# Performance work log

Hardware: AMD Instinct MI355X
Metric: run time of the kernel (lower is better)

Reference implementation:

```python
import jax, jax.numpy as jnp
import numpy as np

LN_EPS = 1e-5


def layer_norm(x, g, b):
    mu = jnp.mean(x, axis=-1, keepdims=True)
    var = jnp.mean(jnp.square(x - mu), axis=-1, keepdims=True)
    return (x - mu) * jax.lax.rsqrt(var + LN_EPS) * g + b


def setup_inputs() -> dict:
    key = jax.random.key(0)
    ks = jax.random.split(key, 8)
    N, E, D = 100000, 1000000, 128
    node_feat = jax.random.normal(ks[0], (N, D), dtype=jnp.float32)
    edge_index = jax.random.randint(ks[1], (2, E), 0, N, dtype=jnp.int64)
    s = 1.0 / np.sqrt(D)
    return {
        "node_feat": node_feat,
        "edge_index": edge_index,
        "layer_idx": 0,
        "ln1_g": jnp.ones((D,), jnp.float32),
        "ln1_b": jnp.zeros((D,), jnp.float32),
        "W_conv": jax.random.normal(ks[2], (D, D), jnp.float32) * s,
        "b_conv": jnp.zeros((D,), jnp.float32),
        "ln2_g": jnp.ones((D,), jnp.float32),
        "ln2_b": jnp.zeros((D,), jnp.float32),
        "W1": jax.random.normal(ks[3], (D, 4 * D), jnp.float32) * s,
        "b1": jnp.zeros((4 * D,), jnp.float32),
        "W2": jax.random.normal(ks[4], (4 * D, D), jnp.float32) * (0.5 * s),
        "b2": jnp.zeros((D,), jnp.float32),
    }


def reference(node_feat, edge_index, layer_idx, ln1_g, ln1_b, W_conv, b_conv,
              ln2_g, ln2_b, W1, b1, W2, b2):
    N = node_feat.shape[0]
    # DeepGCNLayer block='res+': x + conv(dropout(act(norm(x)))); dropout inert at eval
    h = jax.nn.gelu(layer_norm(node_feat, ln1_g, ln1_b), approximate=False)
    # GCNConv: symmetric-normalized aggregation with added self-loops
    hW = h @ W_conv                                         # [N, D]
    loops = jnp.arange(N, dtype=edge_index.dtype)
    src = jnp.concatenate([edge_index[0], loops])           # [E+N]
    dst = jnp.concatenate([edge_index[1], loops])
    deg = jax.ops.segment_sum(jnp.ones(src.shape, hW.dtype), dst, num_segments=N)
    dinv = jnp.where(deg > 0, jax.lax.rsqrt(deg), 0.0)
    coef = dinv[src] * dinv[dst]                            # [E+N]
    agg = jax.ops.segment_sum(hW[src] * coef[:, None], dst, num_segments=N)
    conv_feat = node_feat + agg + b_conv
    # FFN: LN -> Linear(D,4D) -> GELU -> Linear(4D,D) -> GELU, residual from node_feat
    f = layer_norm(conv_feat, ln2_g, ln2_b)
    f = jax.nn.gelu(f @ W1 + b1, approximate=False)
    f = jax.nn.gelu(f @ W2 + b2, approximate=False)
    return node_feat + f
```

## Files before the change

kernel.cpp:

```cpp
#include <hip/hip_runtime.h>
#include <math.h>


typedef _Float16 half8  __attribute__((ext_vector_type(8)));
typedef _Float16 half2v __attribute__((ext_vector_type(2)));
typedef __fp16   fp16x2 __attribute__((ext_vector_type(2)));
typedef float    floatx4 __attribute__((ext_vector_type(4)));

#define SBLK 128

__device__ __forceinline__ float gelu_f(float x){
  float x2 = x*x;
  float z  = x*(1.5957691216f + 0.07135481283f*x2);
  float e  = __expf(-z);
  return x * __builtin_amdgcn_rcpf(1.0f + e);
}
__device__ __forceinline__ unsigned pk16(float a, float b){
  fp16x2 h = __builtin_amdgcn_cvt_pkrtz(a, b);
  return __builtin_bit_cast(unsigned, h);
}
__device__ __forceinline__ float wave_reduce_sum(float v){
  #pragma unroll
  for (int off = 32; off > 0; off >>= 1) v += __shfl_xor(v, off, 64);
  return v;
}

__global__ __launch_bounds__(256) void k_hist(const int* __restrict__ ei, int* __restrict__ cnt,
                                              int E, int NB, int ESB,
    const float* __restrict__ Wc, const float* __restrict__ W1, const float* __restrict__ W2,
    _Float16* __restrict__ Wcp, _Float16* __restrict__ W1p, _Float16* __restrict__ W2p,
    const float* __restrict__ nf, const float* __restrict__ g, const float* __restrict__ b,
    _Float16* __restrict__ hs)
{
  int bid = blockIdx.x;
  if (bid < SBLK){
    __shared__ int h[2048];
    int t = threadIdx.x;
    for (int i = t; i < NB; i += 256) h[i] = 0;
    __syncthreads();
    int e0 = bid * ESB;
    int e1 = min(E, e0 + ESB);
    for (int e = e0 + t; e < e1; e += 256)
      atomicAdd(&h[ei[E + e] >> 6], 1);
    __syncthreads();
    for (int i = t; i < NB; i += 256) cnt[(size_t)bid * NB + i] = h[i];
  } else if (bid < SBLK + 72){
    int id = (bid - SBLK)*256 + threadIdx.x;
    const float* W; _Float16* P; int K, Nc, base;
    if (id < 2048)            { W = Wc; P = Wcp; K = 128; Nc = 128; base = id; }
    else if (id < 2048+8192)  { W = W1; P = W1p; K = 128; Nc = 512; base = id - 2048; }
    else                      { W = W2; P = W2p; K = 512; Nc = 128; base = id - 10240; }
    int lane = base & 63;
    int nkb  = K >> 5;
    int kb   = (base >> 6) % nkb;
    int tile = base / (nkb << 6);
    int col  = (tile << 4) + (lane & 15);
    int k0   = (kb << 5) + ((lane >> 4) << 3);
    _Float16 v[8];
    #pragma unroll
    for (int j = 0; j < 8; j++) v[j] = (_Float16)W[(size_t)(k0 + j)*Nc + col];
    *(half8*)&P[(size_t)base * 8] = *(const half8*)v;
  } else {
    int w = threadIdx.x >> 6, l = threadIdx.x & 63;
    int node = (bid - SBLK - 72)*4 + w;
    float2 x = *(const float2*)&nf[(size_t)node*128 + 2*l];
    float mu = wave_reduce_sum(x.x + x.y) * 0.0078125f;
    float d0 = x.x - mu, d1 = x.y - mu;
    float var = wave_reduce_sum(d0*d0 + d1*d1) * 0.0078125f;
    float rs = rsqrtf(var + 1e-5f);
    float y0 = gelu_f(d0*rs*g[2*l]   + b[2*l]);
    float y1 = gelu_f(d1*rs*g[2*l+1] + b[2*l+1]);
    *(unsigned*)&hs[(size_t)node*128 + 2*l] = pk16(y0, y1);
  }
}

__global__ __launch_bounds__(128) void k_scanB(int* __restrict__ cnt, int* __restrict__ total,
                                               int NB){
  __shared__ int w0sum;
  int b = blockIdx.x;
  int t = threadIdx.x, l = t & 63, w = t >> 6;
  int v = cnt[(size_t)t*NB + b];
  int x = v;
  #pragma unroll
  for (int off = 1; off < 64; off <<= 1){
    int y = __shfl_up(x, off);
    if (l >= off) x += y;
  }
  if (w == 0 && l == 63) w0sum = x;
  __syncthreads();
  int ex = x - v + (w ? w0sum : 0);
  cnt[(size_t)t*NB + b] = ex;
  if (t == 127) total[b] = ex + v;
}

__global__ __launch_bounds__(256) void k_scan2(const int* __restrict__ total,
                                               int* __restrict__ bucketStart, int NB){
  __shared__ int wsum[4];
  int t = threadIdx.x, w = t >> 6, l = t & 63;
  int vals[8];
  int sum = 0;
  #pragma unroll
  for (int j = 0; j < 8; j++){
    int idx = t*8 + j;
    vals[j] = (idx < NB) ? total[idx] : 0;
    sum += vals[j];
  }
  int x = sum;
  #pragma unroll
  for (int off = 1; off < 64; off <<= 1){
    int y = __shfl_up(x, off);
    if (l >= off) x += y;
  }
  if (l == 63) wsum[w] = x;
  __syncthreads();
  if (t == 0){
    int s = 0;
    #pragma unroll
    for (int i = 0; i < 4; i++){ int c = wsum[i]; wsum[i] = s; s += c; }
  }
  __syncthreads();
  int run = wsum[w] + x - sum;
  #pragma unroll
  for (int j = 0; j < 8; j++){
    int idx = t*8 + j;
    if (idx < NB) bucketStart[idx] = run;
    run += vals[j];
  }
  if (t == 255) bucketStart[NB] = run;
}

__global__ __launch_bounds__(256) void k_scatter(const int* __restrict__ ei,
    const int* __restrict__ cnt, const int* __restrict__ bucketStart,
    int* __restrict__ eb, int E, int NB, int ESB){
  __shared__ int cur[2048];
  int t = threadIdx.x;
  for (int i = t; i < NB; i += 256)
    cur[i] = bucketStart[i] + cnt[(size_t)blockIdx.x*NB + i];
  __syncthreads();
  int e0 = blockIdx.x*ESB, e1 = min(E, e0 + ESB);
  for (int e = e0 + t; e < e1; e += 256){
    int s = ei[e], d = ei[E + e];
    int pos = atomicAdd(&cur[d >> 6], 1);
    eb[pos] = (s << 6) | (d & 63);
  }
}

__global__ __launch_bounds__(256) void k_sort2(const int* __restrict__ eb,
    const int* __restrict__ bucketStart, int* __restrict__ eSrc,
    int* __restrict__ row_start, int* __restrict__ incount,
    float* __restrict__ dinv, int N){
  __shared__ int hcnt[64];
  __shared__ int hcur[64];
  int b = blockIdx.x, t = threadIdx.x;
  if (t < 64) hcnt[t] = 0;
  __syncthreads();
  int s0 = bucketStart[b], s1 = bucketStart[b+1];
  for (int e = s0 + t; e < s1; e += 256) atomicAdd(&hcnt[eb[e] & 63], 1);
  __syncthreads();
  if (t < 64){
    int v = hcnt[t];
    int x = v;
    #pragma unroll
    for (int off = 1; off < 64; off <<= 1){
      int y = __shfl_up(x, off);
      if (t >= off) x += y;
    }
    int ex = x - v;
    hcur[t] = ex;
    int node = (b << 6) + t;
    if (node < N){
      row_start[node] = s0 + ex;
      incount[node]   = v;
      dinv[node]      = rsqrtf((float)v + 1.0f);
    }
  }
  __syncthreads();
  for (int e = s0 + t; e < s1; e += 256){
    int v = eb[e];
    int pos = atomicAdd(&hcur[v & 63], 1);
    eSrc[s0 + pos] = v >> 6;
  }
}

__global__ __launch_bounds__(256) void k_gather(const _Float16* __restrict__ hs,
    const int* __restrict__ eSrc, const int* __restrict__ row_start,
    const int* __restrict__ incount, const float* __restrict__ dinv,
    _Float16* __restrict__ aggh, int N)
{
  int w = threadIdx.x >> 6, l = threadIdx.x & 63;
  int node = (blockIdx.x << 2) + w;
  int g  = l >> 3;
  int li = l & 7;
  float dn = dinv[node];
  int start = row_start[node], cnt = incount[node];
  float acc[16];
  #pragma unroll
  for (int i = 0; i < 16; i++) acc[i] = 0.f;
  for (int e = g; e < cnt + 1; e += 8){
    int s = (e == 0) ? node : eSrc[start + e - 1];
    float ds = dinv[s];
    const uint4* hp = (const uint4*)&hs[(size_t)s*128 + (li << 4)];
    uint4 v0 = hp[0], v1 = hp[1];
    half2v p0 = __builtin_bit_cast(half2v, v0.x), p1 = __builtin_bit_cast(half2v, v0.y);
    half2v p2 = __builtin_bit_cast(half2v, v0.z), p3 = __builtin_bit_cast(half2v, v0.w);
    half2v p4 = __builtin_bit_cast(half2v, v1.x), p5 = __builtin_bit_cast(half2v, v1.y);
    half2v p6 = __builtin_bit_cast(half2v, v1.z), p7 = __builtin_bit_cast(half2v, v1.w);
    acc[0]  = fmaf((float)p0.x, ds, acc[0]);  acc[1]  = fmaf((float)p0.y, ds, acc[1]);
    acc[2]  = fmaf((float)p1.x, ds, acc[2]);  acc[3]  = fmaf((float)p1.y, ds, acc[3]);
    acc[4]  = fmaf((float)p2.x, ds, acc[4]);  acc[5]  = fmaf((float)p2.y, ds, acc[5]);
    acc[6]  = fmaf((float)p3.x, ds, acc[6]);  acc[7]  = fmaf((float)p3.y, ds, acc[7]);
    acc[8]  = fmaf((float)p4.x, ds, acc[8]);  acc[9]  = fmaf((float)p4.y, ds, acc[9]);
    acc[10] = fmaf((float)p5.x, ds, acc[10]); acc[11] = fmaf((float)p5.y, ds, acc[11]);
    acc[12] = fmaf((float)p6.x, ds, acc[12]); acc[13] = fmaf((float)p6.y, ds, acc[13]);
    acc[14] = fmaf((float)p7.x, ds, acc[14]); acc[15] = fmaf((float)p7.y, ds, acc[15]);
  }
  #pragma unroll
  for (int i = 0; i < 16; i++){
    acc[i] += __shfl_xor(acc[i], 8);
    acc[i] += __shfl_xor(acc[i], 16);
    acc[i] += __shfl_xor(acc[i], 32);
  }
  if (l < 8){
    uint4 o0, o1;
    o0.x = pk16(dn*acc[0],  dn*acc[1]);  o0.y = pk16(dn*acc[2],  dn*acc[3]);
    o0.z = pk16(dn*acc[4],  dn*acc[5]);  o0.w = pk16(dn*acc[6],  dn*acc[7]);
    o1.x = pk16(dn*acc[8],  dn*acc[9]);  o1.y = pk16(dn*acc[10], dn*acc[11]);
    o1.z = pk16(dn*acc[12], dn*acc[13]); o1.w = pk16(dn*acc[14], dn*acc[15]);
    uint4* op = (uint4*)&aggh[(size_t)node*128 + (l << 4)];
    op[0] = o0; op[1] = o1;
  }
}

__global__ __launch_bounds__(256) void k_ffn(
    const float* __restrict__ nf, const _Float16* __restrict__ aggh,
    const _Float16* __restrict__ Wcp, const float* __restrict__ bc,
    const float* __restrict__ g2, const float* __restrict__ bl2,
    const _Float16* __restrict__ W1p, const float* __restrict__ b1,
    const _Float16* __restrict__ W2p, const float* __restrict__ b2,
    float* __restrict__ out, int N)
{
  __shared__ __align__(16) unsigned short u_s[32*520];
  int t = threadIdx.x, w = t >> 6, l = t & 63;
  int nb = blockIdx.x << 5;
  int quad = l >> 4, ln16 = l & 15;

  {
    int m = t >> 3, c0 = (t & 7) << 4;
    const uint4* src = (const uint4*)&aggh[(size_t)(nb + m)*128 + c0];
    uint4 v0 = src[0], v1 = src[1];
    uint4* dst = (uint4*)&u_s[4352 + m*136 + c0];
    dst[0] = v0; dst[1] = v1;
  }
  __syncthreads();

  {
    half8 ag[2][4];
    #pragma unroll
    for (int mt = 0; mt < 2; mt++)
      #pragma unroll
      for (int kb = 0; kb < 4; kb++)
        ag[mt][kb] = *(const half8*)&u_s[4352 + ((mt << 4) + ln16)*136 + (kb << 5) + (quad << 3)];
    const half8* Wp8 = (const half8*)Wcp;
    #pragma unroll
    for (int nt = 0; nt < 2; nt++){
      int tile = (w << 1) + nt;
      half8 bf[4];
      #pragma unroll
      for (int kb = 0; kb < 4; kb++) bf[kb] = Wp8[(size_t)((tile << 2) + kb)*64 + l];
      floatx4 acc0 = {0.f,0.f,0.f,0.f}, acc1 = {0.f,0.f,0.f,0.f};
      #pragma unroll
      for (int kb = 0; kb < 4; kb++){
        acc0 = __builtin_amdgcn_mfma_f32_16x16x32_f16(ag[0][kb], bf[kb], acc0, 0, 0, 0);
        acc1 = __builtin_amdgcn_mfma_f32_16x16x32_f16(ag[1][kb], bf[kb], acc1, 0, 0, 0);
      }
      int col = (tile << 4) + ln16;
      float bcv = bc[col];
      #pragma unroll
      for (int r = 0; r < 4; r++){
        int m0 = (quad << 2) + r;
        *(_Float16*)&u_s[m0*136 + col]        = (_Float16)(acc0[r] + bcv);
        *(_Float16*)&u_s[(m0 + 16)*136 + col] = (_Float16)(acc1[r] + bcv);
      }
    }
  }
  __syncthreads();

  float2 nfr[8];
  #pragma unroll
  for (int q = 0; q < 8; q++){
    int m = (w << 3) + q;
    unsigned pu = *(unsigned*)&u_s[m*136 + 2*l];
    half2v hp = __builtin_bit_cast(half2v, pu);
    nfr[q] = *(const float2*)&nf[(size_t)(nb + m)*128 + 2*l];
    float x0 = (float)hp.x + nfr[q].x;
    float x1 = (float)hp.y + nfr[q].y;
    float mu = wave_reduce_sum(x0 + x1) * 0.0078125f;
    float d0 = x0 - mu, d1 = x1 - mu;
    float var = wave_reduce_sum(d0*d0 + d1*d1) * 0.0078125f;
    float rs = rsqrtf(var + 1e-5f);
    float y0 = d0*rs*g2[2*l]   + bl2[2*l];
    float y1 = d1*rs*g2[2*l+1] + bl2[2*l+1];
    *(unsigned*)&u_s[m*136 + 2*l] = pk16(y0, y1);
  }
  __syncthreads();

  half8 a[2][4];
  #pragma unroll
  for (int mt = 0; mt < 2; mt++)
    #pragma unroll
    for (int kb = 0; kb < 4; kb++)
      a[mt][kb] = *(const half8*)&u_s[((mt << 4) + ln16)*136 + (kb << 5) + (quad << 3)];
  __syncthreads();

  {
    const half8* Wp8 = (const half8*)W1p;
    #pragma unroll
    for (int nt = 0; nt < 8; nt++){
      int tile = (w << 3) + nt;
      half8 bf[4];
      #pragma unroll
      for (int kb = 0; kb < 4; kb++) bf[kb] = Wp8[(size_t)((tile << 2) + kb)*64 + l];
      floatx4 acc0 = {0.f,0.f,0.f,0.f}, acc1 = {0.f,0.f,0.f,0.f};
      #pragma unroll
      for (int kb = 0; kb < 4; kb++){
        acc0 = __builtin_amdgcn_mfma_f32_16x16x32_f16(a[0][kb], bf[kb], acc0, 0, 0, 0);
        acc1 = __builtin_amdgcn_mfma_f32_16x16x32_f16(a[1][kb], bf[kb], acc1, 0, 0, 0);
      }
      int col = (tile << 4) + ln16;
      float bv = b1[col];
      #pragma unroll
      for (int r = 0; r < 4; r++){
        *(_Float16*)&u_s[((quad << 2) + r)*520 + col]      = (_Float16)gelu_f(acc0[r] + bv);
        *(_Float16*)&u_s[(16 + (quad << 2) + r)*520 + col] = (_Float16)gelu_f(acc1[r] + bv);
      }
    }
  }
  __syncthreads();

  floatx4 acc00 = {0.f,0.f,0.f,0.f}, acc01 = {0.f,0.f,0.f,0.f};
  floatx4 acc10 = {0.f,0.f,0.f,0.f}, acc11 = {0.f,0.f,0.f,0.f};
  int tile0 = (w << 1), tile1 = tile0 + 1;
  {
    const half8* Wp8 = (const half8*)W2p;
    for (int kb = 0; kb < 16; kb++){
      half8 a0 = *(const half8*)&u_s[ln16*520        + (kb << 5) + (quad << 3)];
      half8 a1 = *(const half8*)&u_s[(16 + ln16)*520 + (kb << 5) + (quad << 3)];
      half8 b0  = Wp8[(size_t)((tile0 << 4) + kb)*64 + l];
      half8 b1v = Wp8[(size_t)((tile1 << 4) + kb)*64 + l];
      acc00 = __builtin_amdgcn_mfma_f32_16x16x32_f16(a0, b0,  acc00, 0, 0, 0);
      acc01 = __builtin_amdgcn_mfma_f32_16x16x32_f16(a0, b1v, acc01, 0, 0, 0);
      acc10 = __builtin_amdgcn_mfma_f32_16x16x32_f16(a1, b0,  acc10, 0, 0, 0);
      acc11 = __builtin_amdgcn_mfma_f32_16x16x32_f16(a1, b1v, acc11, 0, 0, 0);
    }
  }
  __syncthreads();

  {
    float* fs = (float*)u_s;
    int col0 = (tile0 << 4) + ln16, col1 = (tile1 << 4) + ln16;
    float bv0 = b2[col0], bv1 = b2[col1];
    #pragma unroll
    for (int r = 0; r < 4; r++){
      int m0 = (quad << 2) + r;
      fs[m0*132 + col0]        = gelu_f(acc00[r] + bv0);
      fs[m0*132 + col1]        = gelu_f(acc01[r] + bv1);
      fs[(m0 + 16)*132 + col0] = gelu_f(acc10[r] + bv0);
      fs[(m0 + 16)*132 + col1] = gelu_f(acc11[r] + bv1);
    }
  }
  __syncthreads();

  {
    const float* fs = (const float*)u_s;
    #pragma unroll
    for (int q = 0; q < 8; q++){
      int m = (w << 3) + q;
      float2 o;
      o.x = nfr[q].x + fs[m*132 + 2*l];
      o.y = nfr[q].y + fs[m*132 + 2*l + 1];
      *(float2*)&out[(size_t)(nb + m)*128 + 2*l] = o;
    }
  }
}

extern "C" void kernel_launch(void* const* d_in, const int* in_sizes, int n_in,
                              void* d_out, int out_size, void* d_ws, size_t ws_size,
                              hipStream_t stream) {
  const float* nf   = (const float*)d_in[0];
  const int*   ei   = (const int*)  d_in[1];
  const float* ln1g = (const float*)d_in[3];
  const float* ln1b = (const float*)d_in[4];
  const float* Wc   = (const float*)d_in[5];
  const float* bc   = (const float*)d_in[6];
  const float* ln2g = (const float*)d_in[7];
  const float* ln2b = (const float*)d_in[8];
  const float* W1   = (const float*)d_in[9];
  const float* b1   = (const float*)d_in[10];
  const float* W2   = (const float*)d_in[11];
  const float* b2   = (const float*)d_in[12];
  float* out = (float*)d_out;

  int N = in_sizes[0] / 128;
  int E = in_sizes[1] / 2;
  int NB  = (N + 63) >> 6;
  int ESB = (E + SBLK - 1) / SBLK;

  char* ws = (char*)d_ws;
  _Float16* hs   = (_Float16*)ws;
  _Float16* aggh = (_Float16*)(ws + (size_t)N*128*2);
  char* p = ws + (size_t)N*128*4;
  p = (char*)(((size_t)p + 15) & ~(size_t)15);
  int*   cnt         = (int*)p;   p += (size_t)SBLK*NB*4;
  int*   total       = (int*)p;   p += (size_t)NB*4;
  int*   bucketStart = (int*)p;   p += (size_t)(NB+1)*4;
  float* dinv        = (float*)p; p += (size_t)N*4;
  int*   incount     = (int*)p;   p += (size_t)N*4;
  int*   row_start   = (int*)p;   p += (size_t)N*4;
  int*   eb          = (int*)p;   p += (size_t)E*4;
  int*   eSrc        = (int*)p;   p += (size_t)E*4;
  p = (char*)(((size_t)p + 15) & ~(size_t)15);
  _Float16* Wcp = (_Float16*)p; p += (size_t)2048*8*2;
  _Float16* W1p = (_Float16*)p; p += (size_t)8192*8*2;
  _Float16* W2p = (_Float16*)p; p += (size_t)8192*8*2;

  k_hist   <<<SBLK + 72 + N/4, 256, 0, stream>>>(ei, cnt, E, NB, ESB,
                                                 Wc, W1, W2, Wcp, W1p, W2p,
                                                 nf, ln1g, ln1b, hs);
  k_scanB  <<<NB, 128, 0, stream>>>(cnt, total, NB);
  k_scan2  <<<1, 256, 0, stream>>>(total, bucketStart, NB);
  k_scatter<<<SBLK, 256, 0, stream>>>(ei, cnt, bucketStart, eb, E, NB, ESB);
  k_sort2  <<<NB, 256, 0, stream>>>(eb, bucketStart, eSrc, row_start, incount, dinv, N);

  k_gather <<<N/4, 256, 0, stream>>>(hs, eSrc, row_start, incount, dinv, aggh, N);
  k_ffn    <<<N/32, 256, 0, stream>>>(nf, aggh, Wcp, bc, ln2g, ln2b, W1p, b1, W2p, b2, out, N);
}
```

Measured before the change: 286.8 us.

## Spread LN1 node blocks across the sort-phase kernels to fill idle CUs

The LayerNorm+GELU work over the N/4 node blocks is split into four fixed chunks (4000/8000/5000/8000), each appended to one of the histogram, per-bucket scan, global scan and scatter kernels. Those small kernels otherwise leave most CUs idle. The per-bucket scan now handles two buckets per 256-thread block, and the weight-packing blocks move into that kernel. The chunk sizes are hardcoded and total exactly N/4 = 25000 for N=100000, so other N would leave nodes uncomputed or read out of range.

After: 289.7 us. Within noise of the previous version (+1.0%).

```diff
diff --git a/kernel.cpp b/kernel.cpp
--- a/kernel.cpp
+++ b/kernel.cpp
@@ -8,6 +8,10 @@
 typedef float    floatx4 __attribute__((ext_vector_type(4)));
 
 #define SBLK 128
+#define LN1_A 4000
+#define LN1_B 8000
+#define LN1_C 5000
+#define LN1_D 8000
 
 __device__ __forceinline__ float gelu_f(float x){
   float x2 = x*x;
@@ -25,10 +29,24 @@
   return v;
 }
 
-__global__ __launch_bounds__(256) void k_hist(const int* __restrict__ ei, int* __restrict__ cnt,
-                                              int E, int NB, int ESB,
-    const float* __restrict__ Wc, const float* __restrict__ W1, const float* __restrict__ W2,
-    _Float16* __restrict__ Wcp, _Float16* __restrict__ W1p, _Float16* __restrict__ W2p,
+__device__ __forceinline__ void ln1_body(int node_blk,
+    const float* __restrict__ nf, const float* __restrict__ g,
+    const float* __restrict__ b, _Float16* __restrict__ hs)
+{
+  int w = threadIdx.x >> 6, l = threadIdx.x & 63;
+  int node = node_blk*4 + w;
+  float2 x = *(const float2*)&nf[(size_t)node*128 + 2*l];
+  float mu = wave_reduce_sum(x.x + x.y) * 0.0078125f;
+  float d0 = x.x - mu, d1 = x.y - mu;
+  float var = wave_reduce_sum(d0*d0 + d1*d1) * 0.0078125f;
+  float rs = rsqrtf(var + 1e-5f);
+  float y0 = gelu_f(d0*rs*g[2*l]   + b[2*l]);
+  float y1 = gelu_f(d1*rs*g[2*l+1] + b[2*l+1]);
+  *(unsigned*)&hs[(size_t)node*128 + 2*l] = pk16(y0, y1);
+}
+
+__global__ __launch_bounds__(256) void kA_hist(const int* __restrict__ ei, int* __restrict__ cnt,
+    int E, int NB, int ESB,
     const float* __restrict__ nf, const float* __restrict__ g, const float* __restrict__ b,
     _Float16* __restrict__ hs)
 {
@@ -44,8 +62,41 @@
       atomicAdd(&h[ei[E + e] >> 6], 1);
     __syncthreads();
     for (int i = t; i < NB; i += 256) cnt[(size_t)bid * NB + i] = h[i];
-  } else if (bid < SBLK + 72){
-    int id = (bid - SBLK)*256 + threadIdx.x;
+  } else {
+    ln1_body(bid - SBLK, nf, g, b, hs);
+  }
+}
+
+__global__ __launch_bounds__(256) void kB_scan(int* __restrict__ cnt, int* __restrict__ total,
+    int NB, int NB2,
+    const float* __restrict__ Wc, const float* __restrict__ W1, const float* __restrict__ W2,
+    _Float16* __restrict__ Wcp, _Float16* __restrict__ W1p, _Float16* __restrict__ W2p,
+    const float* __restrict__ nf, const float* __restrict__ g, const float* __restrict__ b,
+    _Float16* __restrict__ hs)
+{
+  int bid = blockIdx.x;
+  if (bid < NB2){
+    __shared__ int w0s[2];
+    int t = threadIdx.x;
+    int half = t >> 7, tt = t & 127, l = tt & 63, ww = tt >> 6;
+    int bkt = bid*2 + half;
+    bool ok = bkt < NB;
+    int v = ok ? cnt[(size_t)tt*NB + bkt] : 0;
+    int x = v;
+    #pragma unroll
+    for (int off = 1; off < 64; off <<= 1){
+      int y = __shfl_up(x, off);
+      if (l >= off) x += y;
+    }
+    if (ww == 0 && l == 63) w0s[half] = x;
+    __syncthreads();
+    int ex = x - v + (ww ? w0s[half] : 0);
+    if (ok){
+      cnt[(size_t)tt*NB + bkt] = ex;
+      if (tt == 127) total[bkt] = ex + v;
+    }
+  } else if (bid < NB2 + 72){
+    int id = (bid - NB2)*256 + threadIdx.x;
     const float* W; _Float16* P; int K, Nc, base;
     if (id < 2048)            { W = Wc; P = Wcp; K = 128; Nc = 128; base = id; }
     else if (id < 2048+8192)  { W = W1; P = W1p; K = 128; Nc = 512; base = id - 2048; }
@@ -61,87 +112,75 @@
     for (int j = 0; j < 8; j++) v[j] = (_Float16)W[(size_t)(k0 + j)*Nc + col];
     *(half8*)&P[(size_t)base * 8] = *(const half8*)v;
   } else {
-    int w = threadIdx.x >> 6, l = threadIdx.x & 63;
-    int node = (bid - SBLK - 72)*4 + w;
-    float2 x = *(const float2*)&nf[(size_t)node*128 + 2*l];
-    float mu = wave_reduce_sum(x.x + x.y) * 0.0078125f;
-    float d0 = x.x - mu, d1 = x.y - mu;
-    float var = wave_reduce_sum(d0*d0 + d1*d1) * 0.0078125f;
-    float rs = rsqrtf(var + 1e-5f);
-    float y0 = gelu_f(d0*rs*g[2*l]   + b[2*l]);
-    float y1 = gelu_f(d1*rs*g[2*l+1] + b[2*l+1]);
-    *(unsigned*)&hs[(size_t)node*128 + 2*l] = pk16(y0, y1);
-  }
-}
-
-__global__ __launch_bounds__(128) void k_scanB(int* __restrict__ cnt, int* __restrict__ total,
-                                               int NB){
-  __shared__ int w0sum;
-  int b = blockIdx.x;
-  int t = threadIdx.x, l = t & 63, w = t >> 6;
-  int v = cnt[(size_t)t*NB + b];
-  int x = v;
-  #pragma unroll
-  for (int off = 1; off < 64; off <<= 1){
-    int y = __shfl_up(x, off);
-    if (l >= off) x += y;
-  }
-  if (w == 0 && l == 63) w0sum = x;
-  __syncthreads();
-  int ex = x - v + (w ? w0sum : 0);
-  cnt[(size_t)t*NB + b] = ex;
-  if (t == 127) total[b] = ex + v;
-}
-
-__global__ __launch_bounds__(256) void k_scan2(const int* __restrict__ total,
-                                               int* __restrict__ bucketStart, int NB){
-  __shared__ int wsum[4];
-  int t = threadIdx.x, w = t >> 6, l = t & 63;
-  int vals[8];
-  int sum = 0;
-  #pragma unroll
-  for (int j = 0; j < 8; j++){
-    int idx = t*8 + j;
-    vals[j] = (idx < NB) ? total[idx] : 0;
-    sum += vals[j];
-  }
-  int x = sum;
-  #pragma unroll
-  for (int off = 1; off < 64; off <<= 1){
-    int y = __shfl_up(x, off);
-    if (l >= off) x += y;
-  }
-  if (l == 63) wsum[w] = x;
-  __syncthreads();
-  if (t == 0){
-    int s = 0;
-    #pragma unroll
-    for (int i = 0; i < 4; i++){ int c = wsum[i]; wsum[i] = s; s += c; }
-  }
-  __syncthreads();
-  int run = wsum[w] + x - sum;
-  #pragma unroll
-  for (int j = 0; j < 8; j++){
-    int idx = t*8 + j;
-    if (idx < NB) bucketStart[idx] = run;
-    run += vals[j];
-  }
-  if (t == 255) bucketStart[NB] = run;
-}
-
-__global__ __launch_bounds__(256) void k_scatter(const int* __restrict__ ei,
+    ln1_body(LN1_A + (bid - NB2 - 72), nf, g, b, hs);
+  }
+}
+
+__global__ __launch_bounds__(256) void kC_scan2(const int* __restrict__ total,
+    int* __restrict__ bucketStart, int NB,
+    const float* __restrict__ nf, const float* __restrict__ g, const float* __restrict__ b,
+    _Float16* __restrict__ hs)
+{
+  int bid = blockIdx.x;
+  if (bid == 0){
+    __shared__ int wsum[4];
+    int t = threadIdx.x, w = t >> 6, l = t & 63;
+    int vals[8];
+    int sum = 0;
+    #pragma unroll
+    for (int j = 0; j < 8; j++){
+      int idx = t*8 + j;
+      vals[j] = (idx < NB) ? total[idx] : 0;
+      sum += vals[j];
+    }
+    int x = sum;
+    #pragma unroll
+    for (int off = 1; off < 64; off <<= 1){
+      int y = __shfl_up(x, off);
+      if (l >= off) x += y;
+    }
+    if (l == 63) wsum[w] = x;
+    __syncthreads();
+    if (t == 0){
+      int s = 0;
+      #pragma unroll
+      for (int i = 0; i < 4; i++){ int c = wsum[i]; wsum[i] = s; s += c; }
+    }
+    __syncthreads();
+    int run = wsum[w] + x - sum;
+    #pragma unroll
+    for (int j = 0; j < 8; j++){
+      int idx = t*8 + j;
+      if (idx < NB) bucketStart[idx] = run;
+      run += vals[j];
+    }
+    if (t == 255) bucketStart[NB] = run;
+  } else {
+    ln1_body(LN1_A + LN1_B + (bid - 1), nf, g, b, hs);
+  }
+}
+
+__global__ __launch_bounds__(256) void kD_scatter(const int* __restrict__ ei,
     const int* __restrict__ cnt, const int* __restrict__ bucketStart,
-    int* __restrict__ eb, int E, int NB, int ESB){
-  __shared__ int cur[2048];
-  int t = threadIdx.x;
-  for (int i = t; i < NB; i += 256)
-    cur[i] = bucketStart[i] + cnt[(size_t)blockIdx.x*NB + i];
-  __syncthreads();
-  int e0 = blockIdx.x*ESB, e1 = min(E, e0 + ESB);
-  for (int e = e0 + t; e < e1; e += 256){
-    int s = ei[e], d = ei[E + e];
-    int pos = atomicAdd(&cur[d >> 6], 1);
-    eb[pos] = (s << 6) | (d & 63);
+    int* __restrict__ eb, int E, int NB, int ESB,
+    const float* __restrict__ nf, const float* __restrict__ g, const float* __restrict__ b,
+    _Float16* __restrict__ hs)
+{
+  int bid = blockIdx.x;
+  if (bid < SBLK){
+    __shared__ int cur[2048];
+    int t = threadIdx.x;
+    for (int i = t; i < NB; i += 256)
+      cur[i] = bucketStart[i] + cnt[(size_t)bid*NB + i];
+    __syncthreads();
+    int e0 = bid*ESB, e1 = min(E, e0 + ESB);
+    for (int e = e0 + t; e < e1; e += 256){
+      int s = ei[e], d = ei[E + e];
+      int pos = atomicAdd(&cur[d >> 6], 1);
+      eb[pos] = (s << 6) | (d & 63);
+    }
+  } else {
+    ln1_body(LN1_A + LN1_B + LN1_C + (bid - SBLK), nf, g, b, hs);
   }
 }
 
@@ -403,6 +442,7 @@
   int N = in_sizes[0] / 128;
   int E = in_sizes[1] / 2;
   int NB  = (N + 63) >> 6;
+  int NB2 = (NB + 1) >> 1;
   int ESB = (E + SBLK - 1) / SBLK;
 
   char* ws = (char*)d_ws;
@@ -423,14 +463,15 @@
   _Float16* W1p = (_Float16*)p; p += (size_t)8192*8*2;
   _Float16* W2p = (_Float16*)p; p += (size_t)8192*8*2;
 
-  k_hist   <<<SBLK + 72 + N/4, 256, 0, stream>>>(ei, cnt, E, NB, ESB,
-                                                 Wc, W1, W2, Wcp, W1p, W2p,
-                                                 nf, ln1g, ln1b, hs);
-  k_scanB  <<<NB, 128, 0, stream>>>(cnt, total, NB);
-  k_scan2  <<<1, 256, 0, stream>>>(total, bucketStart, NB);
-  k_scatter<<<SBLK, 256, 0, stream>>>(ei, cnt, bucketStart, eb, E, NB, ESB);
-  k_sort2  <<<NB, 256, 0, stream>>>(eb, bucketStart, eSrc, row_start, incount, dinv, N);
-
-  k_gather <<<N/4, 256, 0, stream>>>(hs, eSrc, row_start, incount, dinv, aggh, N);
-  k_ffn    <<<N/32, 256, 0, stream>>>(nf, aggh, Wcp, bc, ln2g, ln2b, W1p, b1, W2p, b2, out, N);
-}
+  kA_hist   <<<SBLK + LN1_A, 256, 0, stream>>>(ei, cnt, E, NB, ESB, nf, ln1g, ln1b, hs);
+  kB_scan   <<<NB2 + 72 + LN1_B, 256, 0, stream>>>(cnt, total, NB, NB2,
+                                                   Wc, W1, W2, Wcp, W1p, W2p,
+                                                   nf, ln1g, ln1b, hs);
+  kC_scan2  <<<1 + LN1_C, 256, 0, stream>>>(total, bucketStart, NB, nf, ln1g, ln1b, hs);
+  kD_scatter<<<SBLK + LN1_D, 256, 0, stream>>>(ei, cnt, bucketStart, eb, E, NB, ESB,
+                                               nf, ln1g, ln1b, hs);
+  k_sort2   <<<NB, 256, 0, stream>>>(eb, bucketStart, eSrc, row_start, incount, dinv, N);
+
+  k_gather  <<<N/4, 256, 0, stream>>>(hs, eSrc, row_start, incount, dinv, aggh, N);
+  k_ffn     <<<N/32, 256, 0, stream>>>(nf, aggh, Wcp, bc, ln2g, ln2b, W1p, b1, W2p, b2, out, N);
+}
```

## Split gather across feature-column slices per block for better cache locality

Applied to the files above, without the earlier changes.

The gather kernel now assigns each block one 16-column slice (32 bytes) of the 128-wide feature rows for 16 nodes, with 8 blocks per node chunk. Each 16-lane group handles one node with 8 edge slots and 2 lanes per slice, so each lane reads one 16-byte vector per edge instead of two. The aim is to shrink per-block working set and raise concurrency and L2 sector reuse across neighbouring blocks. In exchange, edge indices and dinv lookups are re-read 8 times per node, and each load segment is smaller.

Result: slower. 368.0 us (+28.3%).

```diff
diff --git a/kernel.cpp b/kernel.cpp
--- a/kernel.cpp
+++ b/kernel.cpp
@@ -187,47 +187,42 @@
     const int* __restrict__ incount, const float* __restrict__ dinv,
     _Float16* __restrict__ aggh, int N)
 {
-  int w = threadIdx.x >> 6, l = threadIdx.x & 63;
-  int node = (blockIdx.x << 2) + w;
-  int g  = l >> 3;
-  int li = l & 7;
+  int slice = blockIdx.x & 7;
+  int chunk = blockIdx.x >> 3;
+  int t = threadIdx.x, w = t >> 6, l = t & 63;
+  int gl = l & 15;
+  int node = (chunk << 4) + (w << 2) + (l >> 4);
+  int slot = gl >> 1, li = gl & 1;
+  int coff = (slice << 4) + (li << 3);
   float dn = dinv[node];
   int start = row_start[node], cnt = incount[node];
-  float acc[16];
-  #pragma unroll
-  for (int i = 0; i < 16; i++) acc[i] = 0.f;
-  for (int e = g; e < cnt + 1; e += 8){
+  float acc[8];
+  #pragma unroll
+  for (int i = 0; i < 8; i++) acc[i] = 0.f;
+  for (int e = slot; e < cnt + 1; e += 8){
     int s = (e == 0) ? node : eSrc[start + e - 1];
     float ds = dinv[s];
-    const uint4* hp = (const uint4*)&hs[(size_t)s*128 + (li << 4)];
-    uint4 v0 = hp[0], v1 = hp[1];
-    half2v p0 = __builtin_bit_cast(half2v, v0.x), p1 = __builtin_bit_cast(half2v, v0.y);
-    half2v p2 = __builtin_bit_cast(half2v, v0.z), p3 = __builtin_bit_cast(half2v, v0.w);
-    half2v p4 = __builtin_bit_cast(half2v, v1.x), p5 = __builtin_bit_cast(half2v, v1.y);
-    half2v p6 = __builtin_bit_cast(half2v, v1.z), p7 = __builtin_bit_cast(half2v, v1.w);
-    acc[0]  = fmaf((float)p0.x, ds, acc[0]);  acc[1]  = fmaf((float)p0.y, ds, acc[1]);
-    acc[2]  = fmaf((float)p1.x, ds, acc[2]);  acc[3]  = fmaf((float)p1.y, ds, acc[3]);
-    acc[4]  = fmaf((float)p2.x, ds, acc[4]);  acc[5]  = fmaf((float)p2.y, ds, acc[5]);
-    acc[6]  = fmaf((float)p3.x, ds, acc[6]);  acc[7]  = fmaf((float)p3.y, ds, acc[7]);
-    acc[8]  = fmaf((float)p4.x, ds, acc[8]);  acc[9]  = fmaf((float)p4.y, ds, acc[9]);
-    acc[10] = fmaf((float)p5.x, ds, acc[10]); acc[11] = fmaf((float)p5.y, ds, acc[11]);
-    acc[12] = fmaf((float)p6.x, ds, acc[12]); acc[13] = fmaf((float)p6.y, ds, acc[13]);
-    acc[14] = fmaf((float)p7.x, ds, acc[14]); acc[15] = fmaf((float)p7.y, ds, acc[15]);
-  }
-  #pragma unroll
-  for (int i = 0; i < 16; i++){
+    uint4 v = *(const uint4*)&hs[(size_t)s*128 + coff];
+    half2v p0 = __builtin_bit_cast(half2v, v.x), p1 = __builtin_bit_cast(half2v, v.y);
+    half2v p2 = __builtin_bit_cast(half2v, v.z), p3 = __builtin_bit_cast(half2v, v.w);
+    acc[0] = fmaf((float)p0.x, ds, acc[0]); acc[1] = fmaf((float)p0.y, ds, acc[1]);
+    acc[2] = fmaf((float)p1.x, ds, acc[2]); acc[3] = fmaf((float)p1.y, ds, acc[3]);
+    acc[4] = fmaf((float)p2.x, ds, acc[4]); acc[5] = fmaf((float)p2.y, ds, acc[5]);
+    acc[6] = fmaf((float)p3.x, ds, acc[6]); acc[7] = fmaf((float)p3.y, ds, acc[7]);
+  }
+  #pragma unroll
+  for (int i = 0; i < 8; i++){
+    acc[i] += __shfl_xor(acc[i], 2);
+    acc[i] += __shfl_xor(acc[i], 4);
     acc[i] += __shfl_xor(acc[i], 8);
-    acc[i] += __shfl_xor(acc[i], 16);
-    acc[i] += __shfl_xor(acc[i], 32);
-  }
-  if (l < 8){
-    uint4 o0, o1;
-    o0.x = pk16(dn*acc[0],  dn*acc[1]);  o0.y = pk16(dn*acc[2],  dn*acc[3]);
-    o0.z = pk16(dn*acc[4],  dn*acc[5]);  o0.w = pk16(dn*acc[6],  dn*acc[7]);
-    o1.x = pk16(dn*acc[8],  dn*acc[9]);  o1.y = pk16(dn*acc[10], dn*acc[11]);
-    o1.z = pk16(dn*acc[12], dn*acc[13]); o1.w = pk16(dn*acc[14], dn*acc[15]);
-    uint4* op = (uint4*)&aggh[(size_t)node*128 + (l << 4)];
-    op[0] = o0; op[1] = o1;
+  }
+  if (slot == 0){
+    uint4 o;
+    o.x = pk16(dn*acc[0], dn*acc[1]);
+    o.y = pk16(dn*acc[2], dn*acc[3]);
+    o.z = pk16(dn*acc[4], dn*acc[5]);
+    o.w = pk16(dn*acc[6], dn*acc[7]);
+    *(uint4*)&aggh[(size_t)node*128 + coff] = o;
   }
 }
 
@@ -431,6 +426,6 @@
   k_scatter<<<SBLK, 256, 0, stream>>>(ei, cnt, bucketStart, eb, E, NB, ESB);
   k_sort2  <<<NB, 256, 0, stream>>>(eb, bucketStart, eSrc, row_start, incount, dinv, N);
 
-  k_gather <<<N/4, 256, 0, stream>>>(hs, eSrc, row_start, incount, dinv, aggh, N);
+  k_gather <<<(N/16)*8, 256, 0, stream>>>(hs, eSrc, row_start, incount, dinv, aggh, N);
   k_ffn    <<<N/32, 256, 0, stream>>>(nf, aggh, Wcp, bc, ln2g, ln2b, W1p, b1, W2p, b2, out, N);
 }
```

## Replace two-level bucket sort CSR build with global-atomic counting sort

Applied to the files above, without the earlier changes.

Replaces the shared-memory bucket histogram, per-bucket scan, scatter and second-level sort with a direct per-node degree count using global atomics, a three-kernel prefix scan over nodes, and a single fill pass that atomically claims slots per destination node. This removes the intermediate packed edge buffer and the 128xNB count matrix and the two-pass sort. In exchange it relies on many scattered global atomics on the device, and edge order within a row becomes nondeterministic. It also adds an extra zeroing launch.

Result: slower. 363.8 us (+26.9%).

```diff
diff --git a/kernel.cpp b/kernel.cpp
--- a/kernel.cpp
+++ b/kernel.cpp
@@ -7,7 +7,7 @@
 typedef __fp16   fp16x2 __attribute__((ext_vector_type(2)));
 typedef float    floatx4 __attribute__((ext_vector_type(4)));
 
-#define SBLK 128
+#define DEGB 512
 
 __device__ __forceinline__ float gelu_f(float x){
   float x2 = x*x;
@@ -25,27 +25,25 @@
   return v;
 }
 
-__global__ __launch_bounds__(256) void k_hist(const int* __restrict__ ei, int* __restrict__ cnt,
-                                              int E, int NB, int ESB,
+__global__ __launch_bounds__(256) void k_zero(int* __restrict__ deg, int N){
+  int i = blockIdx.x*256 + threadIdx.x;
+  if (i < N) deg[i] = 0;
+}
+
+__global__ __launch_bounds__(256) void kP(const int* __restrict__ ei, int* __restrict__ deg,
+    int E,
     const float* __restrict__ Wc, const float* __restrict__ W1, const float* __restrict__ W2,
     _Float16* __restrict__ Wcp, _Float16* __restrict__ W1p, _Float16* __restrict__ W2p,
     const float* __restrict__ nf, const float* __restrict__ g, const float* __restrict__ b,
     _Float16* __restrict__ hs)
 {
   int bid = blockIdx.x;
-  if (bid < SBLK){
-    __shared__ int h[2048];
-    int t = threadIdx.x;
-    for (int i = t; i < NB; i += 256) h[i] = 0;
-    __syncthreads();
-    int e0 = bid * ESB;
-    int e1 = min(E, e0 + ESB);
-    for (int e = e0 + t; e < e1; e += 256)
-      atomicAdd(&h[ei[E + e] >> 6], 1);
-    __syncthreads();
-    for (int i = t; i < NB; i += 256) cnt[(size_t)bid * NB + i] = h[i];
-  } else if (bid < SBLK + 72){
-    int id = (bid - SBLK)*256 + threadIdx.x;
+  if (bid < DEGB){
+    int stride = DEGB*256;
+    for (int e = bid*256 + threadIdx.x; e < E; e += stride)
+      atomicAdd(&deg[ei[E + e]], 1);
+  } else if (bid < DEGB + 72){
+    int id = (bid - DEGB)*256 + threadIdx.x;
     const float* W; _Float16* P; int K, Nc, base;
     if (id < 2048)            { W = Wc; P = Wcp; K = 128; Nc = 128; base = id; }
     else if (id < 2048+8192)  { W = W1; P = W1p; K = 128; Nc = 512; base = id - 2048; }
@@ -62,7 +60,7 @@
     *(half8*)&P[(size_t)base * 8] = *(const half8*)v;
   } else {
     int w = threadIdx.x >> 6, l = threadIdx.x & 63;
-    int node = (bid - SBLK - 72)*4 + w;
+    int node = (bid - DEGB - 72)*4 + w;
     float2 x = *(const float2*)&nf[(size_t)node*128 + 2*l];
     float mu = wave_reduce_sum(x.x + x.y) * 0.0078125f;
     float d0 = x.x - mu, d1 = x.y - mu;
@@ -74,37 +72,41 @@
   }
 }
 
-__global__ __launch_bounds__(128) void k_scanB(int* __restrict__ cnt, int* __restrict__ total,
-                                               int NB){
-  __shared__ int w0sum;
-  int b = blockIdx.x;
-  int t = threadIdx.x, l = t & 63, w = t >> 6;
-  int v = cnt[(size_t)t*NB + b];
+__global__ __launch_bounds__(256) void kS1(const int* __restrict__ deg,
+    int* __restrict__ row_start, int* __restrict__ bsum, int N)
+{
+  __shared__ int ws4[4];
+  int t = threadIdx.x, w = t >> 6, l = t & 63;
+  int node = blockIdx.x*256 + t;
+  int v = (node < N) ? deg[node] : 0;
   int x = v;
   #pragma unroll
   for (int off = 1; off < 64; off <<= 1){
     int y = __shfl_up(x, off);
     if (l >= off) x += y;
   }
-  if (w == 0 && l == 63) w0sum = x;
-  __syncthreads();
-  int ex = x - v + (w ? w0sum : 0);
-  cnt[(size_t)t*NB + b] = ex;
-  if (t == 127) total[b] = ex + v;
-}
-
-__global__ __launch_bounds__(256) void k_scan2(const int* __restrict__ total,
-                                               int* __restrict__ bucketStart, int NB){
+  if (l == 63) ws4[w] = x;
+  __syncthreads();
+  if (t == 0){
+    int s = 0;
+    #pragma unroll
+    for (int i = 0; i < 4; i++){ int c = ws4[i]; ws4[i] = s; s += c; }
+  }
+  __syncthreads();
+  int ex = ws4[w] + x - v;
+  if (node < N) row_start[node] = ex;
+  if (t == 255) bsum[blockIdx.x] = ex + v;
+}
+
+__global__ __launch_bounds__(256) void kS2(const int* __restrict__ bsum,
+    int* __restrict__ boff, int NBL)
+{
   __shared__ int wsum[4];
   int t = threadIdx.x, w = t >> 6, l = t & 63;
-  int vals[8];
-  int sum = 0;
-  #pragma unroll
-  for (int j = 0; j < 8; j++){
-    int idx = t*8 + j;
-    vals[j] = (idx < NB) ? total[idx] : 0;
-    sum += vals[j];
-  }
+  int i0 = 2*t, i1 = 2*t + 1;
+  int v0 = (i0 < NBL) ? bsum[i0] : 0;
+  int v1 = (i1 < NBL) ? bsum[i1] : 0;
+  int sum = v0 + v1;
   int x = sum;
   #pragma unroll
   for (int off = 1; off < 64; off <<= 1){
@@ -120,65 +122,31 @@
   }
   __syncthreads();
   int run = wsum[w] + x - sum;
-  #pragma unroll
-  for (int j = 0; j < 8; j++){
-    int idx = t*8 + j;
-    if (idx < NB) bucketStart[idx] = run;
-    run += vals[j];
-  }
-  if (t == 255) bucketStart[NB] = run;
-}
-
-__global__ __launch_bounds__(256) void k_scatter(const int* __restrict__ ei,
-    const int* __restrict__ cnt, const int* __restrict__ bucketStart,
-    int* __restrict__ eb, int E, int NB, int ESB){
-  __shared__ int cur[2048];
-  int t = threadIdx.x;
-  for (int i = t; i < NB; i += 256)
-    cur[i] = bucketStart[i] + cnt[(size_t)blockIdx.x*NB + i];
-  __syncthreads();
-  int e0 = blockIdx.x*ESB, e1 = min(E, e0 + ESB);
-  for (int e = e0 + t; e < e1; e += 256){
+  if (i0 < NBL) boff[i0] = run;
+  if (i1 < NBL) boff[i1] = run + v0;
+}
+
+__global__ __launch_bounds__(256) void kS3(const int* __restrict__ deg,
+    int* __restrict__ row_start, int* __restrict__ cur, float* __restrict__ dinv,
+    const int* __restrict__ boff, int N)
+{
+  int node = blockIdx.x*256 + threadIdx.x;
+  if (node < N){
+    int r = row_start[node] + boff[blockIdx.x];
+    row_start[node] = r;
+    cur[node] = r;
+    dinv[node] = rsqrtf((float)deg[node] + 1.0f);
+  }
+}
+
+__global__ __launch_bounds__(256) void kF(const int* __restrict__ ei,
+    int* __restrict__ cur, int* __restrict__ eSrc, int E)
+{
+  int stride = gridDim.x*256;
+  for (int e = blockIdx.x*256 + threadIdx.x; e < E; e += stride){
     int s = ei[e], d = ei[E + e];
-    int pos = atomicAdd(&cur[d >> 6], 1);
-    eb[pos] = (s << 6) | (d & 63);
-  }
-}
-
-__global__ __launch_bounds__(256) void k_sort2(const int* __restrict__ eb,
-    const int* __restrict__ bucketStart, int* __restrict__ eSrc,
-    int* __restrict__ row_start, int* __restrict__ incount,
-    float* __restrict__ dinv, int N){
-  __shared__ int hcnt[64];
-  __shared__ int hcur[64];
-  int b = blockIdx.x, t = threadIdx.x;
-  if (t < 64) hcnt[t] = 0;
-  __syncthreads();
-  int s0 = bucketStart[b], s1 = bucketStart[b+1];
-  for (int e = s0 + t; e < s1; e += 256) atomicAdd(&hcnt[eb[e] & 63], 1);
-  __syncthreads();
-  if (t < 64){
-    int v = hcnt[t];
-    int x = v;
-    #pragma unroll
-    for (int off = 1; off < 64; off <<= 1){
-      int y = __shfl_up(x, off);
-      if (t >= off) x += y;
-    }
-    int ex = x - v;
-    hcur[t] = ex;
-    int node = (b << 6) + t;
-    if (node < N){
-      row_start[node] = s0 + ex;
-      incount[node]   = v;
-      dinv[node]      = rsqrtf((float)v + 1.0f);
-    }
-  }
-  __syncthreads();
-  for (int e = s0 + t; e < s1; e += 256){
-    int v = eb[e];
-    int pos = atomicAdd(&hcur[v & 63], 1);
-    eSrc[s0 + pos] = v >> 6;
+    int pos = atomicAdd(&cur[d], 1);
+    eSrc[pos] = s;
   }
 }
 
@@ -402,35 +370,33 @@
 
   int N = in_sizes[0] / 128;
   int E = in_sizes[1] / 2;
-  int NB  = (N + 63) >> 6;
-  int ESB = (E + SBLK - 1) / SBLK;
+  int NBL = (N + 255) / 256;
 
   char* ws = (char*)d_ws;
   _Float16* hs   = (_Float16*)ws;
   _Float16* aggh = (_Float16*)(ws + (size_t)N*128*2);
   char* p = ws + (size_t)N*128*4;
   p = (char*)(((size_t)p + 15) & ~(size_t)15);
-  int*   cnt         = (int*)p;   p += (size_t)SBLK*NB*4;
-  int*   total       = (int*)p;   p += (size_t)NB*4;
-  int*   bucketStart = (int*)p;   p += (size_t)(NB+1)*4;
-  float* dinv        = (float*)p; p += (size_t)N*4;
-  int*   incount     = (int*)p;   p += (size_t)N*4;
-  int*   row_start   = (int*)p;   p += (size_t)N*4;
-  int*   eb          = (int*)p;   p += (size_t)E*4;
-  int*   eSrc        = (int*)p;   p += (size_t)E*4;
+  int*   deg        = (int*)p;   p += (size_t)N*4;
+  int*   row_start  = (int*)p;   p += (size_t)N*4;
+  int*   cur        = (int*)p;   p += (size_t)N*4;
+  float* dinv       = (float*)p; p += (size_t)N*4;
+  int*   bsum       = (int*)p;   p += (size_t)512*4;
+  int*   boff       = (int*)p;   p += (size_t)512*4;
+  int*   eSrc       = (int*)p;   p += (size_t)E*4;
   p = (char*)(((size_t)p + 15) & ~(size_t)15);
   _Float16* Wcp = (_Float16*)p; p += (size_t)2048*8*2;
   _Float16* W1p = (_Float16*)p; p += (size_t)8192*8*2;
   _Float16* W2p = (_Float16*)p; p += (size_t)8192*8*2;
 
-  k_hist   <<<SBLK + 72 + N/4, 256, 0, stream>>>(ei, cnt, E, NB, ESB,
-                                                 Wc, W1, W2, Wcp, W1p, W2p,
-                                                 nf, ln1g, ln1b, hs);
-  k_scanB  <<<NB, 128, 0, stream>>>(cnt, total, NB);
-  k_scan2  <<<1, 256, 0, stream>>>(total, bucketStart, NB);
-  k_scatter<<<SBLK, 256, 0, stream>>>(ei, cnt, bucketStart, eb, E, NB, ESB);
-  k_sort2  <<<NB, 256, 0, stream>>>(eb, bucketStart, eSrc, row_start, incount, dinv, N);
-
-  k_gather <<<N/4, 256, 0, stream>>>(hs, eSrc, row_start, incount, dinv, aggh, N);
+  k_zero <<<NBL, 256, 0, stream>>>(deg, N);
+  kP  <<<DEGB + 72 + N/4, 256, 0, stream>>>(ei, deg, E, Wc, W1, W2, Wcp, W1p, W2p,
+                                            nf, ln1g, ln1b, hs);
+  kS1 <<<NBL, 256, 0, stream>>>(deg, row_start, bsum, N);
+  kS2 <<<1, 256, 0, stream>>>(bsum, boff, NBL);
+  kS3 <<<NBL, 256, 0, stream>>>(deg, row_start, cur, dinv, boff, N);
+  kF  <<<2048, 256, 0, stream>>>(ei, cur, eSrc, E);
+
+  k_gather <<<N/4, 256, 0, stream>>>(hs, eSrc, row_start, deg, dinv, aggh, N);
   k_ffn    <<<N/32, 256, 0, stream>>>(nf, aggh, Wcp, bc, ln2g, ln2b, W1p, b1, W2p, b2, out, N);
 }
```
